# Performance work log

Measured on AMD Instinct MI355X. Metric: run time of the kernel, lower is better.

The kernel has to match this reference:

```python
import jax, jax.numpy as jnp
import numpy as np

NA, NPA, NT = 4096, 8192, 4096  # authors, papers, terms
HEADS = 8

def _ln(x, g, b):
    m = jnp.mean(x, -1, keepdims=True)
    v = jnp.var(x, -1, keepdims=True)
    return (x - m) * jax.lax.rsqrt(v + 1e-5) * g + b

def _gat(x_src, x_dst, src, dst, W, a_s, a_d, b, n_dst):
    # PyG-style GATConv (shared lin for src/dst, no self loops), per edge type.
    heads, outc = a_s.shape
    h_s = (x_src @ W).reshape(-1, heads, outc)
    h_d = (x_dst @ W).reshape(-1, heads, outc)
    e = jax.nn.leaky_relu(jnp.sum(h_s * a_s, -1)[src] + jnp.sum(h_d * a_d, -1)[dst], 0.2)  # [E,H]
    m = jax.ops.segment_max(e, dst, num_segments=n_dst)
    m = jnp.where(jnp.isfinite(m), m, 0.0)
    w = jnp.exp(e - m[dst])
    den = jax.ops.segment_sum(w, dst, num_segments=n_dst)
    alpha = w / (den[dst] + 1e-16)
    out = jax.ops.segment_sum(h_s[src] * alpha[..., None], dst, num_segments=n_dst)
    return out.reshape(n_dst, heads * outc) + b

def _gtl(x, peQ, peK, db, Wq, bq, Wk, bk, Wv, bv, Wo, bo, g1, be1, Wf1, bf1, Wf2, bf2, g2, be2):
    # PE-modulated dense multi-head attention + FFN, pre/post LN residual blocks.
    N, D = x.shape
    dh = D // HEADS
    Q = (x @ Wq + bq + peQ).reshape(N, HEADS, dh)
    K = (x @ Wk + bk + peK).reshape(N, HEADS, dh)
    V = (x @ Wv + bv).reshape(N, HEADS, dh)
    s = jnp.einsum('nhd,mhd->hnm', Q, K) / jnp.sqrt(jnp.float32(dh)) + db[None, None, :]
    o = jnp.einsum('hnm,mhd->nhd', jax.nn.softmax(s, -1), V).reshape(N, D) @ Wo + bo
    x = _ln(x + o, g1, be1)
    f = jax.nn.relu(x @ Wf1 + bf1) @ Wf2 + bf2
    return _ln(x + f, g2, be2)

def _forward(F, I):
    (x_author, x_paper, x_term, original_A, t1_W, t1_b, t2_W, t2_b, t3_W, t3_b,
     gat1_W, gat1_as, gat1_ad, gat1_b, gat2_W, gat2_as, gat2_ad, gat2_b,
     pe_embed, peWQ, peWK,
     gt_Wq, gt_bq, gt_Wk, gt_bk, gt_Wv, gt_bv, gt_Wo, gt_bo,
     gt_g1, gt_be1, gt_Wf1, gt_bf1, gt_Wf2, gt_bf2, gt_g2, gt_be2,
     cat_W, cat_b, mlp_W1, mlp_b1, mlp_W2, mlp_b2) = F
    (ap_src, ap_dst, pa_src, pa_dst, pt_src, pt_dst, tp_src, tp_dst, deg) = I
    xa = jax.nn.relu(x_author @ t1_W + t1_b)
    xp = jax.nn.relu(x_paper @ t2_W + t2_b)
    xt = jax.nn.relu(x_term @ t3_W + t3_b)
    # to_hetero GAT layer 1 (heads=8, out=128): sum over incoming edge types, relu
    h_p1 = jax.nn.relu(_gat(xa, xp, ap_src, ap_dst, gat1_W[0], gat1_as[0], gat1_ad[0], gat1_b[0], NPA)
                       + _gat(xt, xp, tp_src, tp_dst, gat1_W[3], gat1_as[3], gat1_ad[3], gat1_b[3], NPA))
    h_a1 = jax.nn.relu(_gat(xp, xa, pa_src, pa_dst, gat1_W[1], gat1_as[1], gat1_ad[1], gat1_b[1], NA))
    # layer 2 (heads=1); only author output feeds the graph transformer
    h_a2 = _gat(h_p1, h_a1, pa_src, pa_dst, gat2_W[1], gat2_as[1], gat2_ad[1], gat2_b[1], NA)
    # learned positional encodings + adjacency reconstruction loss
    peQ = pe_embed @ peWQ
    peK = pe_embed @ peWK
    S = jax.nn.sigmoid(peQ @ peK.T)  # [NA, NA]
    loss_pe = jnp.mean((S[None] - original_A) ** 2)
    db = jnp.log(jnp.maximum(deg.astype(jnp.float32), 1.0))  # degree key bias
    x = h_a2
    outs = [x]
    for i in range(gt_Wq.shape[0]):
        x = _gtl(x, peQ, peK, db, gt_Wq[i], gt_bq[i], gt_Wk[i], gt_bk[i], gt_Wv[i], gt_bv[i],
                 gt_Wo[i], gt_bo[i], gt_g1[i], gt_be1[i], gt_Wf1[i], gt_bf1[i], gt_Wf2[i], gt_bf2[i],
                 gt_g2[i], gt_be2[i])
        outs.append(x)
    x_gt = jax.nn.relu(jnp.concatenate(outs, -1) @ cat_W + cat_b)
    logits = jax.nn.relu(x_gt @ mlp_W1 + mlp_b1) @ mlp_W2 + mlp_b2
    return loss_pe, jax.nn.softmax(logits, -1), x_gt

def setup_inputs() -> dict:
    key = jax.random.key(0)
    ks = iter(jax.random.split(key, 100))
    def rn(sh, s=1.0):
        return jax.random.normal(next(ks), sh, jnp.float32) * s
    def ri(sh, hi, lo=0):
        return jax.random.randint(next(ks), sh, lo, hi)
    d = {}
    d['x_author'] = rn((NA, 334)); d['x_paper'] = rn((NPA, 512)); d['x_term'] = rn((NT, 128))
    d['ap_src'] = ri((80000,), NA); d['ap_dst'] = ri((80000,), NPA)
    d['pa_src'] = ri((80000,), NPA); d['pa_dst'] = ri((80000,), NA)
    d['pt_src'] = ri((160000,), NPA); d['pt_dst'] = ri((160000,), NT)
    d['tp_src'] = ri((160000,), NT); d['tp_dst'] = ri((160000,), NPA)
    d['original_A'] = (jax.random.uniform(next(ks), (4, NA, NA)) < 0.005).astype(jnp.float32)
    d['deg'] = ri((NA,), 64, 1)
    p = 0.05
    d['t1_W'] = rn((334, 128), p); d['t1_b'] = jnp.zeros((128,))
    d['t2_W'] = rn((512, 128), p); d['t2_b'] = jnp.zeros((128,))
    d['t3_W'] = rn((128, 128), p); d['t3_b'] = jnp.zeros((128,))
    d['gat1_W'] = rn((4, 128, 1024), p); d['gat1_as'] = rn((4, 8, 128), p)
    d['gat1_ad'] = rn((4, 8, 128), p); d['gat1_b'] = jnp.zeros((4, 1024))
    d['gat2_W'] = rn((4, 1024, 128), p); d['gat2_as'] = rn((4, 1, 128), p)
    d['gat2_ad'] = rn((4, 1, 128), p); d['gat2_b'] = jnp.zeros((4, 128))
    d['pe_embed'] = rn((NA, 128), p); d['peWQ'] = rn((128, 128), p); d['peWK'] = rn((128, 128), p)
    d['gt_Wq'] = rn((2, 128, 128), p); d['gt_bq'] = jnp.zeros((2, 128))
    d['gt_Wk'] = rn((2, 128, 128), p); d['gt_bk'] = jnp.zeros((2, 128))
    d['gt_Wv'] = rn((2, 128, 128), p); d['gt_bv'] = jnp.zeros((2, 128))
    d['gt_Wo'] = rn((2, 128, 128), p); d['gt_bo'] = jnp.zeros((2, 128))
    d['gt_g1'] = jnp.ones((2, 128)); d['gt_be1'] = jnp.zeros((2, 128))
    d['gt_Wf1'] = rn((2, 128, 256), p); d['gt_bf1'] = jnp.zeros((2, 256))
    d['gt_Wf2'] = rn((2, 256, 128), p); d['gt_bf2'] = jnp.zeros((2, 128))
    d['gt_g2'] = jnp.ones((2, 128)); d['gt_be2'] = jnp.zeros((2, 128))
    d['cat_W'] = rn((384, 128), p); d['cat_b'] = jnp.zeros((128,))
    d['mlp_W1'] = rn((128, 256), p); d['mlp_b1'] = jnp.zeros((256,))
    d['mlp_W2'] = rn((256, 4), p); d['mlp_b2'] = jnp.zeros((4,))
    return d

def reference(x_author, x_paper, x_term, ap_src, ap_dst, pa_src, pa_dst, pt_src, pt_dst, tp_src, tp_dst, original_A, deg, t1_W, t1_b, t2_W, t2_b, t3_W, t3_b, gat1_W, gat1_as, gat1_ad, gat1_b, gat2_W, gat2_as, gat2_ad, gat2_b, pe_embed, peWQ, peWK, gt_Wq, gt_bq, gt_Wk, gt_bk, gt_Wv, gt_bv, gt_Wo, gt_bo, gt_g1, gt_be1, gt_Wf1, gt_bf1, gt_Wf2, gt_bf2, gt_g2, gt_be2, cat_W, cat_b, mlp_W1, mlp_b1, mlp_W2, mlp_b2):
    F = (x_author, x_paper, x_term, original_A, t1_W, t1_b, t2_W, t2_b, t3_W, t3_b,
         gat1_W, gat1_as, gat1_ad, gat1_b, gat2_W, gat2_as, gat2_ad, gat2_b,
         pe_embed, peWQ, peWK,
         gt_Wq, gt_bq, gt_Wk, gt_bk, gt_Wv, gt_bv, gt_Wo, gt_bo,
         gt_g1, gt_be1, gt_Wf1, gt_bf1, gt_Wf2, gt_bf2, gt_g2, gt_be2,
         cat_W, cat_b, mlp_W1, mlp_b1, mlp_W2, mlp_b2)
    I = (ap_src, ap_dst, pa_src, pa_dst, pt_src, pt_dst, tp_src, tp_dst, deg)
    return _forward(F, I)
```

## Files before the change

kernel.cpp:

```cpp
#include <hip/hip_runtime.h>
#include <math.h>

#define NA   4096
#define NPA  8192
#define NT   4096
#define E_AP 80000
#define E_PA 80000
#define E_TP 160000
#define E_TOT (E_AP + E_TP + E_PA)
#define NSLOT (NPA + NPA + NA)
#define ASPLIT 4

typedef __attribute__((ext_vector_type(4))) float f32x4;
typedef __attribute__((ext_vector_type(8))) short s16x8;
typedef __attribute__((ext_vector_type(8))) unsigned short u16x8;
typedef unsigned short ushort_t;

__device__ __forceinline__ ushort_t f2bf(float f){
  unsigned u = __float_as_uint(f);
  unsigned r = u + 0x7fffu + ((u >> 16) & 1u);
  return (ushort_t)(r >> 16);
}
__device__ __forceinline__ float bf2f(ushort_t u){
  return __uint_as_float(((unsigned)u) << 16);
}

__global__ __launch_bounds__(256) void gemm_sm4_k(
    const float* __restrict__ A, const float* __restrict__ B, float* __restrict__ C,
    const float* __restrict__ bias, const float* __restrict__ lossAcc, float* __restrict__ lossOut,
    int M, int N, int K, int lda, int ldb, int ldc)
{
  if (blockIdx.x == 0 && threadIdx.x == 0)
    lossOut[0] = lossAcc[0] * (1.0f / 67108864.0f);
  __shared__ float As[16][68];
  __shared__ float Bs[16][68];
  int bm = blockIdx.x * 64, bn = 0;
  int tid = threadIdx.x;
  int tr = tid >> 4, tc = tid & 15;
  float acc[4][4] = {{0.f}};
  for (int k0 = 0; k0 < K; k0 += 16) {
#pragma unroll
    for (int i = 0; i < 4; ++i) {
      int idx = tid + i * 256;
      int r  = idx >> 4, kk = idx & 15;
      int gr = bm + r, gk = k0 + kk;
      As[kk][r] = (gr < M && gk < K) ? A[(size_t)gr * lda + gk] : 0.f;
      int c  = idx & 63, k2 = idx >> 6;
      int gc = bn + c, gk2 = k0 + k2;
      Bs[k2][c] = (gk2 < K && gc < N) ? B[(size_t)gk2 * ldb + gc] : 0.f;
    }
    __syncthreads();
#pragma unroll
    for (int kk = 0; kk < 16; ++kk) {
      float a0[4], b0[4];
#pragma unroll
      for (int i = 0; i < 4; ++i) a0[i] = As[kk][tr * 4 + i];
#pragma unroll
      for (int j = 0; j < 4; ++j) b0[j] = Bs[kk][tc * 4 + j];
#pragma unroll
      for (int i = 0; i < 4; ++i)
#pragma unroll
        for (int j = 0; j < 4; ++j) acc[i][j] = fmaf(a0[i], b0[j], acc[i][j]);
    }
    __syncthreads();
  }
  if (tc != 0) return;
#pragma unroll
  for (int i = 0; i < 4; ++i) {
    int r = bm + tr * 4 + i;
    if (r >= M) continue;
    float l0 = acc[i][0] + bias[0], l1 = acc[i][1] + bias[1];
    float l2 = acc[i][2] + bias[2], l3 = acc[i][3] + bias[3];
    float mx = fmaxf(fmaxf(l0, l1), fmaxf(l2, l3));
    float e0 = __expf(l0 - mx), e1 = __expf(l1 - mx), e2 = __expf(l2 - mx), e3 = __expf(l3 - mx);
    float inv = 1.f / (e0 + e1 + e2 + e3);
    C[(size_t)r * ldc + 0] = e0 * inv;
    C[(size_t)r * ldc + 1] = e1 * inv;
    C[(size_t)r * ldc + 2] = e2 * inv;
    C[(size_t)r * ldc + 3] = e3 * inv;
  }
}

template<int ACT, int TN>
__global__ __launch_bounds__(256) void gemm_mfma_k(
    const void* __restrict__ Ain, const void* __restrict__ A2in, const void* __restrict__ A3in,
    int aBf16,
    const float* __restrict__ B, void* __restrict__ Cout, int cBf16,
    const float* __restrict__ bias,
    const float* __restrict__ addmat, int addCols, int addLd,
    const float* __restrict__ lng, const float* __restrict__ lnb,
    const float* __restrict__ partIn,
    int M, int N, int K, int lda, int ldb, int ldc)
{
  const char* A  = (const char*)Ain;
  const char* A2 = (const char*)A2in;
  const char* A3 = (const char*)A3in;
  char* C = (char*)Cout;

  __shared__ __align__(16) ushort_t As[64][40];
  __shared__ __align__(16) ushort_t Bs[TN][40];
  constexpr int NJ = TN / 32;
  int bm = blockIdx.x * 64, bn = blockIdx.y * TN;
  int tid = threadIdx.x;
  int w = tid >> 6, lane = tid & 63, lg = lane >> 4, lid = lane & 15;
  int wm = (w & 1) * 32, wn = (w >> 1) * (TN / 2);
  f32x4 acc[2][NJ];
#pragma unroll
  for (int i = 0; i < 2; ++i)
#pragma unroll
    for (int j = 0; j < NJ; ++j) acc[i][j] = (f32x4){0.f, 0.f, 0.f, 0.f};

  for (int k0 = 0; k0 < K; k0 += 32) {
    {
      int r = tid >> 2, ks = (tid & 3) * 8;
      u16x8 v;
      if (partIn) {
        int row = bm + r;
        int kcol = k0 + ks;
        int h = kcol >> 4, d0 = kcol & 15;
        float mm = -1e30f;
#pragma unroll
        for (int sp = 0; sp < ASPLIT; ++sp)
          mm = fmaxf(mm, partIn[((size_t)(sp * 8 + h) * NA + row) * 18 + 16]);
        float ll = 0.f;
        float a[8];
#pragma unroll
        for (int j = 0; j < 8; ++j) a[j] = 0.f;
#pragma unroll
        for (int sp = 0; sp < ASPLIT; ++sp) {
          const float* pp = partIn + ((size_t)(sp * 8 + h) * NA + row) * 18;
          float wq = __expf(pp[16] - mm);
          ll += pp[17] * wq;
#pragma unroll
          for (int j = 0; j < 8; ++j) a[j] = fmaf(pp[d0 + j], wq, a[j]);
        }
        float inv = 1.f / ll;
#pragma unroll
        for (int j = 0; j < 8; ++j) v[j] = f2bf(a[j] * inv);
      } else {
        int kcol = k0 + ks;
        const char* Ab = A;
        if (A2) { int seg = kcol >> 7; Ab = (seg == 0) ? A : ((seg == 1) ? A2 : A3); kcol &= 127; }
        if (aBf16) {
          v = *(const u16x8*)((const ushort_t*)Ab + (size_t)(bm + (tid >> 2)) * lda + kcol);
        } else {
          const float* ap = (const float*)Ab + (size_t)(bm + (tid >> 2)) * lda + kcol;
#pragma unroll
          for (int j = 0; j < 8; ++j) {
            int gk = k0 + ks + j;
            float fv = (gk < K) ? ap[j] : 0.f;
            v[j] = f2bf(fv);
          }
        }
      }
      *(u16x8*)&As[tid >> 2][ks] = v;
    }
    if (TN == 128) {
      int n = tid >> 1, ks = (tid & 1) * 16;
      ushort_t tmp[16];
#pragma unroll
      for (int j = 0; j < 16; ++j) {
        int gk = k0 + ks + j;
        float fv = (gk < K) ? B[(size_t)gk * ldb + bn + n] : 0.f;
        tmp[j] = f2bf(fv);
      }
      u16x8 v0, v1;
#pragma unroll
      for (int j = 0; j < 8; ++j) { v0[j] = tmp[j]; v1[j] = tmp[8 + j]; }
      *(u16x8*)&Bs[n][ks] = v0;
      *(u16x8*)&Bs[n][ks + 8] = v1;
// ... 9 lines not shown
      *(u16x8*)&Bs[n][ks] = v;
    }
    __syncthreads();
    s16x8 a_frag[2], b_frag[NJ];
#pragma unroll
    for (int i = 0; i < 2; ++i) a_frag[i] = *(s16x8*)&As[wm + i * 16 + lid][lg * 8];
#pragma unroll
    for (int j = 0; j < NJ; ++j) b_frag[j] = *(s16x8*)&Bs[wn + j * 16 + lid][lg * 8];
#pragma unroll
    for (int i = 0; i < 2; ++i)
#pragma unroll
      for (int j = 0; j < NJ; ++j)
        acc[i][j] = __builtin_amdgcn_mfma_f32_16x16x32_bf16(a_frag[i], b_frag[j], acc[i][j], 0, 0, 0);
    __syncthreads();
  }
  if (ACT == 2) {
    __shared__ float Ct[64][132];
#pragma unroll
    for (int i = 0; i < 2; ++i) {
#pragma unroll
      for (int j = 0; j < NJ; ++j) {
        int coll = wn + j * 16 + lid;
#pragma unroll
        for (int rr = 0; rr < 4; ++rr) {
          int rowl = wm + i * 16 + lg * 4 + rr;
          float v = acc[i][j][rr];
          if (bias) v += bias[coll];
          if (addmat && coll < addCols) v += addmat[(size_t)(bm + rowl) * addLd + coll];
          Ct[rowl][coll] = v;
        }
      }
// ... 6 lines not shown
      float v = Ct[row][part * 32 + c2];
      s += v; q += v * v;
    }
    s += __shfl_xor(s, 1); q += __shfl_xor(q, 1);
    s += __shfl_xor(s, 2); q += __shfl_xor(q, 2);
    float mean = s * (1.f / 128.f);
    float var = q * (1.f / 128.f) - mean * mean;
    float inv = rsqrtf(var + 1e-5f);
    int r = bm + row;
    float* Cf = (float*)C;
#pragma unroll
    for (int c2 = 0; c2 < 32; ++c2) {
      int c = part * 32 + c2;
      Cf[(size_t)r * ldc + c] = (Ct[row][c] - mean) * inv * lng[c] + lnb[c];
    }
  } else {
#pragma unroll
    for (int i = 0; i < 2; ++i) {
#pragma unroll
      for (int j = 0; j < NJ; ++j) {
        int c = bn + wn + j * 16 + lid;
#pragma unroll
        for (int rr = 0; rr < 4; ++rr) {
          int r = bm + wm + i * 16 + lg * 4 + rr;
          float v = acc[i][j][rr];
          if (bias)   v += bias[c];
          if (addmat && c < addCols) v += addmat[(size_t)r * addLd + c];
          if (ACT == 1) v = fmaxf(v, 0.f);
          if (cBf16) ((ushort_t*)C)[(size_t)r * ldc + c] = f2bf(v);
          else       ((float*)C)[(size_t)r * ldc + c] = v;
// ... 104 lines not shown
        else       ((float*)C)[(size_t)r * ldc + c] = v;
      }
    }
  }
}

__global__ void prep_k(const float* __restrict__ gat1_b, const float* __restrict__ gat1_W,
                       const float* __restrict__ Wq, const float* __restrict__ bq,
                       const float* __restrict__ Wk, const float* __restrict__ bk,
                       const float* __restrict__ Wv, const float* __restrict__ bv,
                       const float* __restrict__ peWQ, const float* __restrict__ peWK,
                       const int* __restrict__ deg,
                       const float* __restrict__ gat1_as, const float* __restrict__ gat1_ad,
                       const int* __restrict__ ap_dst, const int* __restrict__ tp_dst,
                       const int* __restrict__ pa_dst,
                       float* __restrict__ bsum, float* __restrict__ Wqkv,
                       float* __restrict__ bqkv, float* __restrict__ peW,
                       float* __restrict__ Bstack, float* __restrict__ dbv,
                       float* __restrict__ Ps, float* __restrict__ Pd,
                       int* __restrict__ cnt)
{
  int idx = blockIdx.x * blockDim.x + threadIdx.x;
  if (idx < 1024) { bsum[idx] = gat1_b[idx] + gat1_b[3 * 1024 + idx]; return; }
  idx -= 1024;
  if (idx < 2 * 128 * 384) {
    int l = idx / 49152, rem = idx % 49152;
    int k = rem / 384, c = rem % 384;
    float v;
    if (c < 128)      v = Wq[(size_t)l * 16384 + k * 128 + c];
    else if (c < 256) v = Wk[(size_t)l * 16384 + k * 128 + c - 128];
    else              v = Wv[(size_t)l * 16384 + k * 128 + c - 256];
    Wqkv[(size_t)l * 49152 + k * 384 + c] = v;
    return;
  }
  idx -= 2 * 128 * 384;
// ... 30 lines not shown
    const float* a1 = gat1_as + wsel[type] * 1024 + h * 128;
    const float* a2 = gat1_ad + wsel[type] * 1024 + h * 128;
    float s1 = 0.f, s2 = 0.f;
    for (int c = 0; c < 128; ++c){ float wv = wr[c]; s1 = fmaf(wv, a1[c], s1); s2 = fmaf(wv, a2[c], s2); }
    Ps[(size_t)type * 1024 + k * 8 + h] = s1;
    Pd[(size_t)type * 1024 + k * 8 + h] = s2;
    return;
  }
  idx -= 3 * 1024;
  if (idx < E_TOT) {
    int slot;
    if (idx < E_AP)             slot = ap_dst[idx];
    else if (idx < E_AP + E_TP) slot = NPA + tp_dst[idx - E_AP];
    else                        slot = 2 * NPA + pa_dst[idx - E_AP - E_TP];
    atomicAdd(&cnt[slot], 1);
  }
}

__global__ void scatterf_k(const int* __restrict__ ap_dst, const int* __restrict__ tp_dst,
                           const int* __restrict__ pa_dst, const int* __restrict__ off,
                           int* __restrict__ cur, int* __restrict__ eidx){
  int i = blockIdx.x * blockDim.x + threadIdx.x;
  if (i >= E_TOT) return;
  int slot, local;
  if (i < E_AP)             { local = i;                 slot = ap_dst[local]; }
  else if (i < E_AP + E_TP) { local = i - E_AP;          slot = NPA + tp_dst[local]; }
  else                      { local = i - E_AP - E_TP;   slot = 2 * NPA + pa_dst[local]; }
  int p = atomicAdd(&cur[slot], 1);
  eidx[off[slot] + p] = local;
}
// ... 129 lines not shown
    float mn = fmaxf(mh, v);
    float sc = __expf(mh - mn);
    float w_ = __expf(v - mn);
    den = den * sc + w_;
    mh = mn;
    unsigned u = *(const unsigned*)(hs + (size_t)s * 128 + 2 * lane);
    a0 = fmaf(w_, bf2f((ushort_t)(u & 0xffff)), a0 * sc);
    a1 = fmaf(w_, bf2f((ushort_t)(u >> 16)), a1 * sc);
    e = en; s = sn;
  }
  float inv = 1.f / (den + 1e-16f);
  outp[(size_t)d * 128 + 2 * lane]     = a0 * inv + bias[2 * lane];
  outp[(size_t)d * 128 + 2 * lane + 1] = a1 * inv + bias[2 * lane + 1];
}

__global__ __launch_bounds__(256) void rowdot2_k(const ushort_t* __restrict__ X,
    const float* __restrict__ va, const float* __restrict__ vb, float* __restrict__ out){
  int r = blockIdx.x * 4 + (threadIdx.x >> 6);
  int lane = threadIdx.x & 63;
  const float* v = (r < 8192) ? va : vb;
  unsigned u = *(const unsigned*)(X + (size_t)r * 128 + 2 * lane);
  float s = bf2f((ushort_t)(u & 0xffff)) * v[2 * lane]
          + bf2f((ushort_t)(u >> 16)) * v[2 * lane + 1];
#pragma unroll
  for (int o = 32; o; o >>= 1) s += __shfl_down(s, o);
  if (lane == 0) out[r] = s;
}

__global__ __launch_bounds__(256) void loss_mfma_k(const float* __restrict__ peQ,
    const float* __restrict__ peK, const float* __restrict__ A4, float* __restrict__ lossAcc)
{
  __shared__ __align__(16) ushort_t As[64][40];
  __shared__ __align__(16) ushort_t Bs[128][40];
  __shared__ float sig[64][128];
  __shared__ float red[256];
  int br = blockIdx.x * 64, bc = blockIdx.y * 128;
  int tid = threadIdx.x;
  int w = tid >> 6, lane = tid & 63, lg = lane >> 4, lid = lane & 15;
  int wm = (w & 1) * 32, wn = (w >> 1) * 64;
  f32x4 acc[2][4];
#pragma unroll
  for (int i = 0; i < 2; ++i)
#pragma unroll
// ... 154 lines not shown
      s16x8 pa = *(s16x8*)&Pl[w][lid][32 * kc + 8 * lg];
      s16x8 vb = *(s16x8*)&Vt[lid][32 * kc + 8 * lg];
      o = __builtin_amdgcn_mfma_f32_16x16x32_bf16(pa, vb, o, 0, 0, 0);
    }
  }
  float* pb = part + ((size_t)(sp * 8 + h) * NA) * 18;
#pragma unroll
  for (int r = 0; r < 4; ++r) {
    int qq = qbase + 16 * w + 4 * lg + r;
    pb[(size_t)qq * 18 + lid] = o[r];
  }
  if (lg == 0) {
    int qq = qbase + 16 * w + lid;
    pb[(size_t)qq * 18 + 16] = m;
    pb[(size_t)qq * 18 + 17] = l;
  }
}

__global__ void setval_k(float* p, float v){ p[0] = v; }

extern "C" void kernel_launch(void* const* d_in, const int* in_sizes, int n_in,
                              void* d_out, int out_size, void* d_ws, size_t ws_size,
                              hipStream_t stream)
{
  (void)in_sizes; (void)n_in; (void)out_size;
  const float* x_author = (const float*)d_in[0];
  const float* x_paper  = (const float*)d_in[1];
  const float* x_term   = (const float*)d_in[2];
  const int* ap_src = (const int*)d_in[3];
  const int* ap_dst = (const int*)d_in[4];
// ... 45 lines not shown
  ushort_t* agg  = (ushort_t*)alloc((size_t)NSLOT * 1024 * 2);
  float* scores = (float*)alloc((size_t)36864 * 8 * 4);
  float* Ps   = (float*)alloc(3 * 1024 * 4);
  float* Pd   = (float*)alloc(3 * 1024 * 4);
  ushort_t* hs2 = (ushort_t*)alloc((size_t)NPA * 128 * 2);
  ushort_t* hd2 = (ushort_t*)alloc((size_t)NA * 128 * 2);
  float* s2sd = (float*)alloc((size_t)(NPA + NA) * 4);
  float* hA2  = (float*)alloc((size_t)NA * 128 * 4);
  float* peQK = (float*)alloc((size_t)NA * 256 * 4);
  float* dbv  = (float*)alloc((size_t)NA * 4);
  float* bsum = (float*)alloc(1024 * 4);
  float* Wqkv = (float*)alloc((size_t)2 * 128 * 384 * 4);
  float* bqkv = (float*)alloc((size_t)2 * 384 * 4);
  float* peW  = (float*)alloc((size_t)128 * 256 * 4);
  float* Bstack = (float*)alloc((size_t)256 * 1024 * 4);
  ushort_t* QKVb = (ushort_t*)alloc((size_t)NA * 384 * 2);
  float* x1b  = (float*)alloc((size_t)NA * 128 * 4);
  ushort_t* f1 = (ushort_t*)alloc((size_t)NA * 256 * 2);
  float* outs1= (float*)alloc((size_t)NA * 128 * 4);
  float* outs2= (float*)alloc((size_t)NA * 128 * 4);
  float* l1   = (float*)alloc((size_t)NA * 256 * 4);
  int*   offb = (int*)alloc((size_t)NSLOT * 4);
  int*   eidx = (int*)alloc((size_t)E_TOT * 4);
  size_t zstart = off;
  int*      cnt   = (int*)alloc((size_t)NSLOT * 4);
  int*      cur   = (int*)alloc((size_t)NSLOT * 4);
  float*    lossAcc = (float*)alloc(256);
  size_t zlen = off - zstart;

  float* part = (float*)accP;

  if (off > ws_size){
    setval_k<<<1, 1, 0, stream>>>(out, -12345.0f);
    return;
  }

  auto gemmx = [&](int act, int tn, const void* A, const void* A2, const void* A3, int aBf16,
                   const float* B, void* C, int cBf16, const float* bias,
                   const float* addmat, int addCols, int addLd,
                   const float* lng, const float* lnb, const float* partIn,
                   int M, int N, int K, int lda, int ldb, int ldc){
    dim3 g(M / 64, N / tn, 1);
    if (tn == 128) {
      if (act == 0)      gemm_mfma_k<0,128><<<g, 256, 0, stream>>>(A, A2, A3, aBf16, B, C, cBf16, bias, addmat, addCols, addLd, lng, lnb, partIn, M, N, K, lda, ldb, ldc);
      else if (act == 1) gemm_mfma_k<1,128><<<g, 256, 0, stream>>>(A, A2, A3, aBf16, B, C, cBf16, bias, addmat, addCols, addLd, lng, lnb, partIn, M, N, K, lda, ldb, ldc);
      else               gemm_mfma_k<2,128><<<g, 256, 0, stream>>>(A, A2, A3, aBf16, B, C, cBf16, bias, addmat, addCols, addLd, lng, lnb, partIn, M, N, K, lda, ldb, ldc);
    } else {
      if (act == 0)      gemm_mfma_k<0,64><<<g, 256, 0, stream>>>(A, A2, A3, aBf16, B, C, cBf16, bias, addmat, addCols, addLd, lng, lnb, partIn, M, N, K, lda, ldb, ldc);
      else               gemm_mfma_k<1,64><<<g, 256, 0, stream>>>(A, A2, A3, aBf16, B, C, cBf16, bias, addmat, addCols, addLd, lng, lnb, partIn, M, N, K, lda, ldb, ldc);
    }
  };

  hipMemsetAsync(base + zstart, 0, zlen, stream);
  prep_k<<<2822, 256, 0, stream>>>(gat1_b, gat1_W, gt_Wq, gt_bq, gt_Wk, gt_bk, gt_Wv, gt_bv,
                                   peWQ, peWK, deg, gat1_as, gat1_ad, ap_dst, tp_dst, pa_dst,
                                   bsum, Wqkv, bqkv, peW, Bstack, dbv, Ps, Pd, cnt);
  {
    GDescArr da; da.nd = 4;
    da.d[0] = { x_author, nullptr, t1_W, xa, t1_b, 0, 1, 1, NA, 128, 334, 334, 128, 128, 1, 0, 0, 0, 0 };
    da.d[1] = { x_paper,  nullptr, t2_W, xp, t2_b, 0, 1, 1, NPA, 128, 512, 512, 128, 128, 1, 0, 0, 0, 128 };
    da.d[2] = { x_term,   nullptr, t3_W, xt, t3_b, 0, 1, 1, NT, 128, 128, 128, 128, 128, 1, 0, 0, 0, 384 };
    da.d[3] = { pe_embed, nullptr, peW, peQK, nullptr, 0, 0, 0, NA, 256, 128, 128, 256, 256, 1, 0, 0, 0, 512 };
    gemm_multi_k<<<768, 256, 0, stream>>>(da);
  }
  exscan_k<<<1, 1024, 0, stream>>>(cnt, offb, NSLOT);
  scatterf_k<<<(E_TOT + 255) / 256, 256, 0, stream>>>(ap_dst, tp_dst, pa_dst, offb, cur, eidx);
  scorev_k<<<9216, 256, 0, stream>>>(xa, xp, xt, Ps, Pd, scores);
  agg8ff_k<<<NSLOT / 4, 256, 0, stream>>>(eidx, offb, cnt, ap_src, tp_src, pa_src,
                                          xa, xt, xp, scores, agg);
  {
    GDescArr da; da.nd = 2;
    da.d[0] = { agg, agg + (size_t)NPA * 1024, Bstack, accP, bsum, 1, 1, 1,
                NPA, 128, 256, 1024, 1024, 1024, 8, 128, 128, 128, 0 };
    da.d[1] = { agg + (size_t)2 * NPA * 1024, nullptr, gat1_W + 131072, accA, gat1_b + 1024, 1, 1, 1,
                NA, 128, 128, 1024, 1024, 1024, 8, 128, 128, 128, 2048 };
    gemm_multi_k<<<3072, 256, 0, stream>>>(da);
  }
  gemmx(0, 64, accP, 0, 0, 1, gat2_W + 131072, hs2, 1, 0, 0, 0, 0, 0, 0, 0,
        NPA + NA, 128, 1024, 1024, 128, 128);
  rowdot2_k<<<(NPA + NA) / 4, 256, 0, stream>>>(hs2, gat2_as + 128, gat2_ad + 128, s2sd);
  gat_agg1f_k<<<NA / 4, 256, 0, stream>>>(eidx, offb + 2 * NPA, cnt + 2 * NPA, pa_src, hs2, s2sd,
                                          gat2_b + 128, hA2, NA);
  loss_mfma_k<<<dim3(64, 32), 256, 0, stream>>>(peQK, peQK + 128, original_A, lossAcc);
  const float* x = hA2;
  float* louts[2] = { outs1, outs2 };
  for (int i = 0; i < 2; ++i){
    const float* Wo = gt_Wo + i * 16384; const float* bo = gt_bo + i * 128;
    const float* Wf1 = gt_Wf1 + i * 32768; const float* bf1 = gt_bf1 + i * 256;
    const float* Wf2 = gt_Wf2 + i * 32768; const float* bf2 = gt_bf2 + i * 128;
    gemmx(0, 64, x, 0, 0, 0, Wqkv + (size_t)i * 49152, QKVb, 1, bqkv + i * 384, peQK, 256, 256,
          0, 0, 0, NA, 384, 128, 128, 384, 384);
    attn_mfma_k<<<dim3(NA / 64, 8, ASPLIT), 256, 0, stream>>>(QKVb, QKVb + 128, QKVb + 256, dbv, part);
    gemmx(2, 128, nullptr, 0, 0, 0, Wo, x1b, 0, bo, x, 128, 128, gt_g1 + i * 128, gt_be1 + i * 128,
          part, NA, 128, 128, 128, 128, 128);
    gemmx(1, 64, x1b, 0, 0, 0, Wf1, f1, 1, bf1, 0, 0, 0, 0, 0, 0, NA, 256, 128, 128, 256, 256);
    gemmx(2, 128, f1, 0, 0, 1, Wf2, louts[i], 0, bf2, x1b, 128, 128, gt_g2 + i * 128, gt_be2 + i * 128,
          0, NA, 128, 256, 256, 128, 128);
    x = louts[i];
  }
  float* xgt = out + 1 + NA * 4;
  gemmx(1, 64, hA2, outs1, outs2, 0, cat_W, xgt, 0, cat_b, 0, 0, 0, 0, 0, 0,
        NA, 128, 384, 128, 128, 128);
  gemmx(1, 64, xgt, 0, 0, 0, mlp_W1, l1, 0, mlp_b1, 0, 0, 0, 0, 0, 0, NA, 256, 128, 128, 256, 256);
  gemm_sm4_k<<<64, 256, 0, stream>>>(l1, mlp_W2, out + 1, mlp_b2, lossAcc, out, NA, 4, 256, 256, 4, 4);
}
```

Measured before the change: 777.4 us.

## Fuse transformer tail and MLP head into single kernels with pre-transposed bf16 weights

Each transformer layer's output projection, first LayerNorm, FFN and second LayerNorm now run in one kernel over 16-row tiles, keeping intermediates in shared memory. The concat/MLP head is fused the same way, including the final softmax. The GAT2 row-dot is folded into the GEMM epilogue, and weights are pre-transposed to bf16 in the prep kernel. This removes several launches and global round trips, at the cost of 16-row tiles that reuse weights less and launch only 256 blocks per kernel.

```diff
diff --git a/kernel.cpp b/kernel.cpp
--- a/kernel.cpp
+++ b/kernel.cpp
@@ -25,62 +25,6 @@
   return __uint_as_float(((unsigned)u) << 16);
 }
 
-__global__ __launch_bounds__(256) void gemm_sm4_k(
-    const float* __restrict__ A, const float* __restrict__ B, float* __restrict__ C,
-    const float* __restrict__ bias, const float* __restrict__ lossAcc, float* __restrict__ lossOut,
-    int M, int N, int K, int lda, int ldb, int ldc)
-{
-  if (blockIdx.x == 0 && threadIdx.x == 0)
-    lossOut[0] = lossAcc[0] * (1.0f / 67108864.0f);
-  __shared__ float As[16][68];
-  __shared__ float Bs[16][68];
-  int bm = blockIdx.x * 64, bn = 0;
-  int tid = threadIdx.x;
-  int tr = tid >> 4, tc = tid & 15;
-  float acc[4][4] = {{0.f}};
-  for (int k0 = 0; k0 < K; k0 += 16) {
-#pragma unroll
-    for (int i = 0; i < 4; ++i) {
-      int idx = tid + i * 256;
-      int r  = idx >> 4, kk = idx & 15;
-      int gr = bm + r, gk = k0 + kk;
-      As[kk][r] = (gr < M && gk < K) ? A[(size_t)gr * lda + gk] : 0.f;
-      int c  = idx & 63, k2 = idx >> 6;
-      int gc = bn + c, gk2 = k0 + k2;
-      Bs[k2][c] = (gk2 < K && gc < N) ? B[(size_t)gk2 * ldb + gc] : 0.f;
-    }
-    __syncthreads();
-#pragma unroll
-    for (int kk = 0; kk < 16; ++kk) {
-      float a0[4], b0[4];
-#pragma unroll
-      for (int i = 0; i < 4; ++i) a0[i] = As[kk][tr * 4 + i];
-#pragma unroll
-      for (int j = 0; j < 4; ++j) b0[j] = Bs[kk][tc * 4 + j];
-#pragma unroll
-      for (int i = 0; i < 4; ++i)
-#pragma unroll
-        for (int j = 0; j < 4; ++j) acc[i][j] = fmaf(a0[i], b0[j], acc[i][j]);
-    }
-    __syncthreads();
-  }
-  if (tc != 0) return;
-#pragma unroll
-  for (int i = 0; i < 4; ++i) {
-    int r = bm + tr * 4 + i;
-    if (r >= M) continue;
-    float l0 = acc[i][0] + bias[0], l1 = acc[i][1] + bias[1];
-    float l2 = acc[i][2] + bias[2], l3 = acc[i][3] + bias[3];
-    float mx = fmaxf(fmaxf(l0, l1), fmaxf(l2, l3));
-    float e0 = __expf(l0 - mx), e1 = __expf(l1 - mx), e2 = __expf(l2 - mx), e3 = __expf(l3 - mx);
-    float inv = 1.f / (e0 + e1 + e2 + e3);
-    C[(size_t)r * ldc + 0] = e0 * inv;
-    C[(size_t)r * ldc + 1] = e1 * inv;
-    C[(size_t)r * ldc + 2] = e2 * inv;
-    C[(size_t)r * ldc + 3] = e3 * inv;
-  }
-}
-
 template<int ACT, int TN>
 __global__ __launch_bounds__(256) void gemm_mfma_k(
     const void* __restrict__ Ain, const void* __restrict__ A2in, const void* __restrict__ A3in,
@@ -89,7 +33,7 @@
     const float* __restrict__ bias,
     const float* __restrict__ addmat, int addCols, int addLd,
     const float* __restrict__ lng, const float* __restrict__ lnb,
-    const float* __restrict__ partIn,
+    float* __restrict__ rdOut,
     int M, int N, int K, int lda, int ldb, int ldc)
 {
   const char* A  = (const char*)Ain;
@@ -113,47 +57,22 @@
   for (int k0 = 0; k0 < K; k0 += 32) {
     {
       int r = tid >> 2, ks = (tid & 3) * 8;
+      int kcol = k0 + ks;
+      const char* Ab = A;
+      if (A2) { int seg = kcol >> 7; Ab = (seg == 0) ? A : ((seg == 1) ? A2 : A3); kcol &= 127; }
       u16x8 v;
-      if (partIn) {
-        int row = bm + r;
-        int kcol = k0 + ks;
-        int h = kcol >> 4, d0 = kcol & 15;
-        float mm = -1e30f;
-#pragma unroll
-        for (int sp = 0; sp < ASPLIT; ++sp)
-          mm = fmaxf(mm, partIn[((size_t)(sp * 8 + h) * NA + row) * 18 + 16]);
-        float ll = 0.f;
-        float a[8];
-#pragma unroll
-        for (int j = 0; j < 8; ++j) a[j] = 0.f;
-#pragma unroll
-        for (int sp = 0; sp < ASPLIT; ++sp) {
-          const float* pp = partIn + ((size_t)(sp * 8 + h) * NA + row) * 18;
-          float wq = __expf(pp[16] - mm);
-          ll += pp[17] * wq;
-#pragma unroll
-          for (int j = 0; j < 8; ++j) a[j] = fmaf(pp[d0 + j], wq, a[j]);
-        }
-        float inv = 1.f / ll;
-#pragma unroll
-        for (int j = 0; j < 8; ++j) v[j] = f2bf(a[j] * inv);
+      if (aBf16) {
+        v = *(const u16x8*)((const ushort_t*)Ab + (size_t)(bm + r) * lda + kcol);
       } else {
-        int kcol = k0 + ks;
-        const char* Ab = A;
-        if (A2) { int seg = kcol >> 7; Ab = (seg == 0) ? A : ((seg == 1) ? A2 : A3); kcol &= 127; }
-        if (aBf16) {
-          v = *(const u16x8*)((const ushort_t*)Ab + (size_t)(bm + (tid >> 2)) * lda + kcol);
-        } else {
-          const float* ap = (const float*)Ab + (size_t)(bm + (tid >> 2)) * lda + kcol;
-#pragma unroll
-          for (int j = 0; j < 8; ++j) {
-            int gk = k0 + ks + j;
-            float fv = (gk < K) ? ap[j] : 0.f;
-            v[j] = f2bf(fv);
-          }
+        const float* ap = (const float*)Ab + (size_t)(bm + r) * lda + kcol;
+#pragma unroll
+        for (int j = 0; j < 8; ++j) {
+          int gk = k0 + ks + j;
+          float fv = (gk < K) ? ap[j] : 0.f;
+          v[j] = f2bf(fv);
         }
       }
-      *(u16x8*)&As[tid >> 2][ks] = v;
+      *(u16x8*)&As[r][ks] = v;
     }
     if (TN == 128) {
       int n = tid >> 1, ks = (tid & 1) * 16;
@@ -193,7 +112,7 @@
         acc[i][j] = __builtin_amdgcn_mfma_f32_16x16x32_bf16(a_frag[i], b_frag[j], acc[i][j], 0, 0, 0);
     __syncthreads();
   }
-  if (ACT == 2) {
+  if constexpr (ACT == 2) {
     __shared__ float Ct[64][132];
 #pragma unroll
     for (int i = 0; i < 2; ++i) {
@@ -230,6 +149,35 @@
       int c = part * 32 + c2;
       Cf[(size_t)r * ldc + c] = (Ct[row][c] - mean) * inv * lng[c] + lnb[c];
     }
+  } else if constexpr (ACT == 3) {
+    __shared__ float Ct[64][132];
+#pragma unroll
+    for (int i = 0; i < 2; ++i) {
+#pragma unroll
+      for (int j = 0; j < NJ; ++j) {
+        int coll = wn + j * 16 + lid;
+#pragma unroll
+        for (int rr = 0; rr < 4; ++rr) {
+          int rowl = wm + i * 16 + lg * 4 + rr;
+          Ct[rowl][coll] = acc[i][j][rr];
+        }
+      }
+    }
+    __syncthreads();
+    int row = tid >> 2, part = tid & 3;
+    const float* vsel = (bm + row < 8192) ? lng : lnb;
+    float rd = 0.f;
+    ushort_t* Cu = (ushort_t*)C;
+#pragma unroll
+    for (int c2 = 0; c2 < 32; ++c2) {
+      int c = part * 32 + c2;
+      float f = Ct[row][c];
+      rd = fmaf(f, vsel[c], rd);
+      Cu[(size_t)(bm + row) * ldc + c] = f2bf(f);
+    }
+    rd += __shfl_xor(rd, 1);
+    rd += __shfl_xor(rd, 2);
+    if (part == 0) rdOut[bm + row] = rd;
   } else {
 #pragma unroll
     for (int i = 0; i < 2; ++i) {
@@ -364,11 +312,17 @@
                        const float* __restrict__ gat1_as, const float* __restrict__ gat1_ad,
                        const int* __restrict__ ap_dst, const int* __restrict__ tp_dst,
                        const int* __restrict__ pa_dst,
+                       const float* __restrict__ gt_Wo, const float* __restrict__ gt_Wf1,
+                       const float* __restrict__ gt_Wf2, const float* __restrict__ cat_W,
+                       const float* __restrict__ mlp_W1,
                        float* __restrict__ bsum, float* __restrict__ Wqkv,
                        float* __restrict__ bqkv, float* __restrict__ peW,
                        float* __restrict__ Bstack, float* __restrict__ dbv,
                        float* __restrict__ Ps, float* __restrict__ Pd,
-                       int* __restrict__ cnt)
+                       int* __restrict__ cnt,
+                       ushort_t* __restrict__ Wot, ushort_t* __restrict__ Wf1t,
+                       ushort_t* __restrict__ Wf2t, ushort_t* __restrict__ catt,
+                       ushort_t* __restrict__ mlp1t)
 {
   int idx = blockIdx.x * blockDim.x + threadIdx.x;
   if (idx < 1024) { bsum[idx] = gat1_b[idx] + gat1_b[3 * 1024 + idx]; return; }
@@ -429,6 +383,39 @@
     else if (idx < E_AP + E_TP) slot = NPA + tp_dst[idx - E_AP];
     else                        slot = 2 * NPA + pa_dst[idx - E_AP - E_TP];
     atomicAdd(&cnt[slot], 1);
+    return;
+  }
+  idx -= E_TOT;
+  if (idx < 2 * 128 * 128) {
+    int l = idx / 16384, rem = idx % 16384;
+    int n = rem / 128, k = rem % 128;
+    Wot[idx] = f2bf(gt_Wo[(size_t)l * 16384 + k * 128 + n]);
+    return;
+  }
+  idx -= 2 * 128 * 128;
+  if (idx < 2 * 256 * 128) {
+    int l = idx / 32768, rem = idx % 32768;
+    int n = rem / 128, k = rem % 128;
+    Wf1t[idx] = f2bf(gt_Wf1[(size_t)l * 32768 + k * 256 + n]);
+    return;
+  }
+  idx -= 2 * 256 * 128;
+  if (idx < 2 * 128 * 256) {
+    int l = idx / 32768, rem = idx % 32768;
+    int n = rem / 256, k = rem % 256;
+    Wf2t[idx] = f2bf(gt_Wf2[(size_t)l * 32768 + k * 128 + n]);
+    return;
+  }
+  idx -= 2 * 128 * 256;
+  if (idx < 128 * 384) {
+    int n = idx / 384, k = idx % 384;
+    catt[idx] = f2bf(cat_W[(size_t)k * 128 + n]);
+    return;
+  }
+  idx -= 128 * 384;
+  if (idx < 256 * 128) {
+    int n = idx / 128, k = idx % 128;
+    mlp1t[idx] = f2bf(mlp_W1[(size_t)k * 256 + n]);
   }
 }
 
@@ -588,19 +575,6 @@
   outp[(size_t)d * 128 + 2 * lane + 1] = a1 * inv + bias[2 * lane + 1];
 }
 
-__global__ __launch_bounds__(256) void rowdot2_k(const ushort_t* __restrict__ X,
-    const float* __restrict__ va, const float* __restrict__ vb, float* __restrict__ out){
-  int r = blockIdx.x * 4 + (threadIdx.x >> 6);
-  int lane = threadIdx.x & 63;
-  const float* v = (r < 8192) ? va : vb;
-  unsigned u = *(const unsigned*)(X + (size_t)r * 128 + 2 * lane);
-  float s = bf2f((ushort_t)(u & 0xffff)) * v[2 * lane]
-          + bf2f((ushort_t)(u >> 16)) * v[2 * lane + 1];
-#pragma unroll
-  for (int o = 32; o; o >>= 1) s += __shfl_down(s, o);
-  if (lane == 0) out[r] = s;
-}
-
 __global__ __launch_bounds__(256) void loss_mfma_k(const float* __restrict__ peQ,
     const float* __restrict__ peK, const float* __restrict__ A4, float* __restrict__ lossAcc)
 {
@@ -785,6 +759,270 @@
     int qq = qbase + 16 * w + lid;
     pb[(size_t)qq * 18 + 16] = m;
     pb[(size_t)qq * 18 + 17] = l;
+  }
+}
+
+__global__ __launch_bounds__(256) void gt_tail_k(
+    const float* __restrict__ part,
+    const ushort_t* __restrict__ Wot, const float* __restrict__ bo,
+    const float* __restrict__ xin,
+    const float* __restrict__ g1, const float* __restrict__ be1,
+    const ushort_t* __restrict__ Wf1t, const float* __restrict__ bf1,
+    const ushort_t* __restrict__ Wf2t, const float* __restrict__ bf2,
+    const float* __restrict__ g2, const float* __restrict__ be2,
+    float* __restrict__ outX)
+{
+  __shared__ __align__(16) ushort_t Aly[16][136];
+  __shared__ __align__(16) ushort_t Bs[256][40];
+  __shared__ __align__(16) ushort_t F1b[16][264];
+  __shared__ float X1[16][132];
+  int bm = blockIdx.x * 16;
+  int tid = threadIdx.x;
+  int w = tid >> 6, lane = tid & 63, lg = lane >> 4, lid = lane & 15;
+
+  {
+    int row = bm + (tid >> 4);
+    int seg = tid & 15;
+    int kcol = seg * 8;
+    int h = kcol >> 4, d0 = kcol & 15;
+    float mm = -1e30f;
+#pragma unroll
+    for (int sp = 0; sp < ASPLIT; ++sp)
+      mm = fmaxf(mm, part[((size_t)(sp * 8 + h) * NA + row) * 18 + 16]);
+    float ll = 0.f, a[8];
+#pragma unroll
+    for (int j = 0; j < 8; ++j) a[j] = 0.f;
+#pragma unroll
+    for (int sp = 0; sp < ASPLIT; ++sp){
+      const float* pp = part + ((size_t)(sp * 8 + h) * NA + row) * 18;
+      float wq = __expf(pp[16] - mm);
+      ll += pp[17] * wq;
+#pragma unroll
+      for (int j = 0; j < 8; ++j) a[j] = fmaf(pp[d0 + j], wq, a[j]);
+    }
+    float inv = 1.f / ll;
+    u16x8 v;
+#pragma unroll
+    for (int j = 0; j < 8; ++j) v[j] = f2bf(a[j] * inv);
+    *(u16x8*)&Aly[tid >> 4][kcol] = v;
+  }
+  __syncthreads();
+
+  f32x4 acc1[2];
+  acc1[0] = (f32x4){0.f,0.f,0.f,0.f};
+  acc1[1] = (f32x4){0.f,0.f,0.f,0.f};
+  for (int k0 = 0; k0 < 128; k0 += 32){
+    int n = tid >> 1, ks = (tid & 1) * 16;
+    *(u16x8*)&Bs[n][ks]     = *(const u16x8*)(Wot + (size_t)n * 128 + k0 + ks);
+    *(u16x8*)&Bs[n][ks + 8] = *(const u16x8*)(Wot + (size_t)n * 128 + k0 + ks + 8);
+    __syncthreads();
+    s16x8 af = *(s16x8*)&Aly[lid][k0 + lg * 8];
+#pragma unroll
+    for (int j = 0; j < 2; ++j){
+      s16x8 bf = *(s16x8*)&Bs[w * 32 + j * 16 + lid][lg * 8];
+      acc1[j] = __builtin_amdgcn_mfma_f32_16x16x32_bf16(af, bf, acc1[j], 0, 0, 0);
+    }
+    __syncthreads();
+  }
+#pragma unroll
+  for (int j = 0; j < 2; ++j)
+#pragma unroll
+    for (int rr = 0; rr < 4; ++rr){
+      int r = lg * 4 + rr, c = w * 32 + j * 16 + lid;
+      X1[r][c] = acc1[j][rr] + bo[c] + xin[(size_t)(bm + r) * 128 + c];
+    }
+  __syncthreads();
+  {
+    int r = tid >> 4, p = tid & 15;
+    float s = 0.f, q = 0.f;
+#pragma unroll
+    for (int j = 0; j < 8; ++j){ float v = X1[r][p * 8 + j]; s += v; q += v * v; }
+#pragma unroll
+    for (int mk = 1; mk < 16; mk <<= 1){ s += __shfl_xor(s, mk); q += __shfl_xor(q, mk); }
+    float mean = s * (1.f / 128.f), var = q * (1.f / 128.f) - mean * mean;
+    float inv = rsqrtf(var + 1e-5f);
+    u16x8 v;
+#pragma unroll
+    for (int j = 0; j < 8; ++j){
+      int c = p * 8 + j;
+      float f = (X1[r][c] - mean) * inv * g1[c] + be1[c];
+      X1[r][c] = f;
+      v[j] = f2bf(f);
+    }
+    *(u16x8*)&Aly[r][p * 8] = v;
+  }
+  __syncthreads();
+
+  f32x4 acc2[4];
+#pragma unroll
+  for (int j = 0; j < 4; ++j) acc2[j] = (f32x4){0.f,0.f,0.f,0.f};
+  for (int k0 = 0; k0 < 128; k0 += 32){
+#pragma unroll
+    for (int q4 = 0; q4 < 4; ++q4)
+      *(u16x8*)&Bs[tid][q4 * 8] = *(const u16x8*)(Wf1t + (size_t)tid * 128 + k0 + q4 * 8);
+    __syncthreads();
+    s16x8 af = *(s16x8*)&Aly[lid][k0 + lg * 8];
+#pragma unroll
+    for (int j = 0; j < 4; ++j){
+      s16x8 bf = *(s16x8*)&Bs[w * 64 + j * 16 + lid][lg * 8];
+      acc2[j] = __builtin_amdgcn_mfma_f32_16x16x32_bf16(af, bf, acc2[j], 0, 0, 0);
+    }
+    __syncthreads();
+  }
+#pragma unroll
+  for (int j = 0; j < 4; ++j)
+#pragma unroll
+    for (int rr = 0; rr < 4; ++rr){
+      int r = lg * 4 + rr, c = w * 64 + j * 16 + lid;
+      F1b[r][c] = f2bf(fmaxf(acc2[j][rr] + bf1[c], 0.f));
+    }
+  __syncthreads();
+
+  f32x4 acc3[2];
+  acc3[0] = (f32x4){0.f,0.f,0.f,0.f};
+  acc3[1] = (f32x4){0.f,0.f,0.f,0.f};
+  for (int k0 = 0; k0 < 256; k0 += 32){
+    int n = tid >> 1, ks = (tid & 1) * 16;
+    *(u16x8*)&Bs[n][ks]     = *(const u16x8*)(Wf2t + (size_t)n * 256 + k0 + ks);
+    *(u16x8*)&Bs[n][ks + 8] = *(const u16x8*)(Wf2t + (size_t)n * 256 + k0 + ks + 8);
+    __syncthreads();
+    s16x8 af = *(s16x8*)&F1b[lid][k0 + lg * 8];
+#pragma unroll
+    for (int j = 0; j < 2; ++j){
+      s16x8 bf = *(s16x8*)&Bs[w * 32 + j * 16 + lid][lg * 8];
+      acc3[j] = __builtin_amdgcn_mfma_f32_16x16x32_bf16(af, bf, acc3[j], 0, 0, 0);
+    }
+    __syncthreads();
+  }
+#pragma unroll
+  for (int j = 0; j < 2; ++j)
+#pragma unroll
+    for (int rr = 0; rr < 4; ++rr){
+      int r = lg * 4 + rr, c = w * 32 + j * 16 + lid;
+      X1[r][c] = acc3[j][rr] + bf2[c] + X1[r][c];
+    }
+  __syncthreads();
+  {
+    int r = tid >> 4, p = tid & 15;
+    float s = 0.f, q = 0.f;
+#pragma unroll
+    for (int j = 0; j < 8; ++j){ float v = X1[r][p * 8 + j]; s += v; q += v * v; }
+#pragma unroll
+    for (int mk = 1; mk < 16; mk <<= 1){ s += __shfl_xor(s, mk); q += __shfl_xor(q, mk); }
+    float mean = s * (1.f / 128.f), var = q * (1.f / 128.f) - mean * mean;
+    float inv = rsqrtf(var + 1e-5f);
+#pragma unroll
+    for (int j = 0; j < 8; ++j){
+      int c = p * 8 + j;
+      outX[(size_t)(bm + r) * 128 + c] = (X1[r][c] - mean) * inv * g2[c] + be2[c];
+    }
+  }
+}
+
+__global__ __launch_bounds__(256) void head_k(
+    const float* __restrict__ hA2, const float* __restrict__ o1, const float* __restrict__ o2,
+    const ushort_t* __restrict__ catt, const float* __restrict__ cat_b,
+    const ushort_t* __restrict__ mlp1t, const float* __restrict__ mlp_b1,
+    const float* __restrict__ mlp_W2, const float* __restrict__ mlp_b2,
+    const float* __restrict__ lossAcc, float* __restrict__ out)
+{
+  __shared__ __align__(16) ushort_t Aly[16][392];
+  __shared__ __align__(16) ushort_t Bs[256][40];
+  __shared__ __align__(16) ushort_t L1b[16][264];
+  __shared__ float LG[16][4];
+  int bm = blockIdx.x * 16;
+  int tid = threadIdx.x;
+  int w = tid >> 6, lane = tid & 63, lg = lane >> 4, lid = lane & 15;
+  if (blockIdx.x == 0 && tid == 0) out[0] = lossAcc[0] * (1.0f / 67108864.0f);
+
+  {
+    int r = bm + (tid >> 4), seg = tid & 15;
+#pragma unroll
+    for (int ch = 0; ch < 3; ++ch){
+      int c0 = seg * 24 + ch * 8;
+      const float* src; int cc;
+      if (c0 < 128)      { src = hA2; cc = c0; }
+      else if (c0 < 256) { src = o1;  cc = c0 - 128; }
+      else               { src = o2;  cc = c0 - 256; }
+      u16x8 v;
+#pragma unroll
+      for (int j = 0; j < 8; ++j) v[j] = f2bf(src[(size_t)r * 128 + cc + j]);
+      *(u16x8*)&Aly[tid >> 4][c0] = v;
+    }
+  }
+  __syncthreads();
+
+  float* xgt = out + 1 + NA * 4;
+  f32x4 acc1[2];
+  acc1[0] = (f32x4){0.f,0.f,0.f,0.f};
+  acc1[1] = (f32x4){0.f,0.f,0.f,0.f};
+  for (int k0 = 0; k0 < 384; k0 += 32){
+    int n = tid >> 1, ks = (tid & 1) * 16;
+    *(u16x8*)&Bs[n][ks]     = *(const u16x8*)(catt + (size_t)n * 384 + k0 + ks);
+    *(u16x8*)&Bs[n][ks + 8] = *(const u16x8*)(catt + (size_t)n * 384 + k0 + ks + 8);
+    __syncthreads();
+    s16x8 af = *(s16x8*)&Aly[lid][k0 + lg * 8];
+#pragma unroll
+    for (int j = 0; j < 2; ++j){
+      s16x8 bf = *(s16x8*)&Bs[w * 32 + j * 16 + lid][lg * 8];
+      acc1[j] = __builtin_amdgcn_mfma_f32_16x16x32_bf16(af, bf, acc1[j], 0, 0, 0);
+    }
+    __syncthreads();
+  }
+#pragma unroll
+  for (int j = 0; j < 2; ++j)
+#pragma unroll
+    for (int rr = 0; rr < 4; ++rr){
+      int r = lg * 4 + rr, c = w * 32 + j * 16 + lid;
+      float f = fmaxf(acc1[j][rr] + cat_b[c], 0.f);
+      xgt[(size_t)(bm + r) * 128 + c] = f;
+      Aly[r][c] = f2bf(f);
+    }
+  __syncthreads();
+
+  f32x4 acc2[4];
+#pragma unroll
+  for (int j = 0; j < 4; ++j) acc2[j] = (f32x4){0.f,0.f,0.f,0.f};
+  for (int k0 = 0; k0 < 128; k0 += 32){
+#pragma unroll
+    for (int q4 = 0; q4 < 4; ++q4)
+      *(u16x8*)&Bs[tid][q4 * 8] = *(const u16x8*)(mlp1t + (size_t)tid * 128 + k0 + q4 * 8);
+    __syncthreads();
+    s16x8 af = *(s16x8*)&Aly[lid][k0 + lg * 8];
+#pragma unroll
+    for (int j = 0; j < 4; ++j){
+      s16x8 bf = *(s16x8*)&Bs[w * 64 + j * 16 + lid][lg * 8];
+      acc2[j] = __builtin_amdgcn_mfma_f32_16x16x32_bf16(af, bf, acc2[j], 0, 0, 0);
+    }
+    __syncthreads();
+  }
+#pragma unroll
+  for (int j = 0; j < 4; ++j)
+#pragma unroll
+    for (int rr = 0; rr < 4; ++rr){
+      int r = lg * 4 + rr, c = w * 64 + j * 16 + lid;
+      L1b[r][c] = f2bf(fmaxf(acc2[j][rr] + mlp_b1[c], 0.f));
+    }
+  __syncthreads();
+
+  {
+    int r = tid >> 4, rem = tid & 15, c = rem >> 2, p = rem & 3;
+    float s = 0.f;
+    for (int k = p * 64; k < p * 64 + 64; ++k)
+      s = fmaf(bf2f(L1b[r][k]), mlp_W2[(size_t)k * 4 + c], s);
+    s += __shfl_xor(s, 1);
+    s += __shfl_xor(s, 2);
+    if (p == 0) LG[r][c] = s + mlp_b2[c];
+  }
+  __syncthreads();
+  if (tid < 16){
+    int r = tid;
+    float l0 = LG[r][0], l1 = LG[r][1], l2 = LG[r][2], l3 = LG[r][3];
+    float mx = fmaxf(fmaxf(l0, l1), fmaxf(l2, l3));
+    float e0 = __expf(l0 - mx), e1 = __expf(l1 - mx), e2 = __expf(l2 - mx), e3 = __expf(l3 - mx);
+    float inv = 1.f / (e0 + e1 + e2 + e3);
+    float* o = out + 1 + (size_t)(bm + r) * 4;
+    o[0] = e0 * inv; o[1] = e1 * inv; o[2] = e2 * inv; o[3] = e3 * inv;
   }
 }
 
@@ -860,12 +1098,14 @@
   float* bqkv = (float*)alloc((size_t)2 * 384 * 4);
   float* peW  = (float*)alloc((size_t)128 * 256 * 4);
   float* Bstack = (float*)alloc((size_t)256 * 1024 * 4);
+  ushort_t* Wot   = (ushort_t*)alloc((size_t)2 * 128 * 128 * 2);
+  ushort_t* Wf1t  = (ushort_t*)alloc((size_t)2 * 256 * 128 * 2);
+  ushort_t* Wf2t  = (ushort_t*)alloc((size_t)2 * 128 * 256 * 2);
+  ushort_t* catt  = (ushort_t*)alloc((size_t)128 * 384 * 2);
+  ushort_t* mlp1t = (ushort_t*)alloc((size_t)256 * 128 * 2);
   ushort_t* QKVb = (ushort_t*)alloc((size_t)NA * 384 * 2);
-  float* x1b  = (float*)alloc((size_t)NA * 128 * 4);
-  ushort_t* f1 = (ushort_t*)alloc((size_t)NA * 256 * 2);
   float* outs1= (float*)alloc((size_t)NA * 128 * 4);
   float* outs2= (float*)alloc((size_t)NA * 128 * 4);
-  float* l1   = (float*)alloc((size_t)NA * 256 * 4);
   int*   offb = (int*)alloc((size_t)NSLOT * 4);
   int*   eidx = (int*)alloc((size_t)E_TOT * 4);
   size_t zstart = off;
@@ -884,23 +1124,26 @@
   auto gemmx = [&](int act, int tn, const void* A, const void* A2, const void* A3, int aBf16,
                    const float* B, void* C, int cBf16, const float* bias,
                    const float* addmat, int addCols, int addLd,
-                   const float* lng, const float* lnb, const float* partIn,
+                   const float* lng, const float* lnb, float* rdOut,
                    int M, int N, int K, int lda, int ldb, int ldc){
     dim3 g(M / 64, N / tn, 1);
     if (tn == 128) {
-      if (act == 0)      gemm_mfma_k<0,128><<<g, 256, 0, stream>>>(A, A2, A3, aBf16, B, C, cBf16, bias, addmat, addCols, addLd, lng, lnb, partIn, M, N, K, lda, ldb, ldc);
-      else if (act == 1) gemm_mfma_k<1,128><<<g, 256, 0, stream>>>(A, A2, A3, aBf16, B, C, cBf16, bias, addmat, addCols, addLd, lng, lnb, partIn, M, N, K, lda, ldb, ldc);
-      else               gemm_mfma_k<2,128><<<g, 256, 0, stream>>>(A, A2, A3, aBf16, B, C, cBf16, bias, addmat, addCols, addLd, lng, lnb, partIn, M, N, K, lda, ldb, ldc);
+      if (act == 0)      gemm_mfma_k<0,128><<<g, 256, 0, stream>>>(A, A2, A3, aBf16, B, C, cBf16, bias, addmat, addCols, addLd, lng, lnb, rdOut, M, N, K, lda, ldb, ldc);
+      else if (act == 1) gemm_mfma_k<1,128><<<g, 256, 0, stream>>>(A, A2, A3, aBf16, B, C, cBf16, bias, addmat, addCols, addLd, lng, lnb, rdOut, M, N, K, lda, ldb, ldc);
+      else if (act == 2) gemm_mfma_k<2,128><<<g, 256, 0, stream>>>(A, A2, A3, aBf16, B, C, cBf16, bias, addmat, addCols, addLd, lng, lnb, rdOut, M, N, K, lda, ldb, ldc);
+      else               gemm_mfma_k<3,128><<<g, 256, 0, stream>>>(A, A2, A3, aBf16, B, C, cBf16, bias, addmat, addCols, addLd, lng, lnb, rdOut, M, N, K, lda, ldb, ldc);
     } else {
-      if (act == 0)      gemm_mfma_k<0,64><<<g, 256, 0, stream>>>(A, A2, A3, aBf16, B, C, cBf16, bias, addmat, addCols, addLd, lng, lnb, partIn, M, N, K, lda, ldb, ldc);
-      else               gemm_mfma_k<1,64><<<g, 256, 0, stream>>>(A, A2, A3, aBf16, B, C, cBf16, bias, addmat, addCols, addLd, lng, lnb, partIn, M, N, K, lda, ldb, ldc);
+      if (act == 0)      gemm_mfma_k<0,64><<<g, 256, 0, stream>>>(A, A2, A3, aBf16, B, C, cBf16, bias, addmat, addCols, addLd, lng, lnb, rdOut, M, N, K, lda, ldb, ldc);
+      else               gemm_mfma_k<1,64><<<g, 256, 0, stream>>>(A, A2, A3, aBf16, B, C, cBf16, bias, addmat, addCols, addLd, lng, lnb, rdOut, M, N, K, lda, ldb, ldc);
     }
   };
 
   hipMemsetAsync(base + zstart, 0, zlen, stream);
-  prep_k<<<2822, 256, 0, stream>>>(gat1_b, gat1_W, gt_Wq, gt_bq, gt_Wk, gt_bk, gt_Wv, gt_bv,
+  prep_k<<<3781, 256, 0, stream>>>(gat1_b, gat1_W, gt_Wq, gt_bq, gt_Wk, gt_bk, gt_Wv, gt_bv,
                                    peWQ, peWK, deg, gat1_as, gat1_ad, ap_dst, tp_dst, pa_dst,
-                                   bsum, Wqkv, bqkv, peW, Bstack, dbv, Ps, Pd, cnt);
+                                   gt_Wo, gt_Wf1, gt_Wf2, cat_W, mlp_W1,
+                                   bsum, Wqkv, bqkv, peW, Bstack, dbv, Ps, Pd, cnt,
+                                   Wot, Wf1t, Wf2t, catt, mlp1t);
   {
     GDescArr da; da.nd = 4;
     da.d[0] = { x_author, nullptr, t1_W, xa, t1_b, 0, 1, 1, NA, 128, 334, 334, 128, 128, 1, 0, 0, 0, 0 };
@@ -922,31 +1165,24 @@
                 NA, 128, 128, 1024, 1024, 1024, 8, 128, 128, 128, 2048 };
     gemm_multi_k<<<3072, 256, 0, stream>>>(da);
   }
-  gemmx(0, 64, accP, 0, 0, 1, gat2_W + 131072, hs2, 1, 0, 0, 0, 0, 0, 0, 0,
-        NPA + NA, 128, 1024, 1024, 128, 128);
-  rowdot2_k<<<(NPA + NA) / 4, 256, 0, stream>>>(hs2, gat2_as + 128, gat2_ad + 128, s2sd);
+  gemmx(3, 128, accP, 0, 0, 1, gat2_W + 131072, hs2, 1, 0, 0, 0, 0,
+        gat2_as + 128, gat2_ad + 128, s2sd, NPA + NA, 128, 1024, 1024, 128, 128);
   gat_agg1f_k<<<NA / 4, 256, 0, stream>>>(eidx, offb + 2 * NPA, cnt + 2 * NPA, pa_src, hs2, s2sd,
                                           gat2_b + 128, hA2, NA);
   loss_mfma_k<<<dim3(64, 32), 256, 0, stream>>>(peQK, peQK + 128, original_A, lossAcc);
   const float* x = hA2;
   float* louts[2] = { outs1, outs2 };
   for (int i = 0; i < 2; ++i){
-    const float* Wo = gt_Wo + i * 16384; const float* bo = gt_bo + i * 128;
-    const float* Wf1 = gt_Wf1 + i * 32768; const float* bf1 = gt_bf1 + i * 256;
-    const float* Wf2 = gt_Wf2 + i * 32768; const float* bf2 = gt_bf2 + i * 128;
     gemmx(0, 64, x, 0, 0, 0, Wqkv + (size_t)i * 49152, QKVb, 1, bqkv + i * 384, peQK, 256, 256,
           0, 0, 0, NA, 384, 128, 128, 384, 384);
     attn_mfma_k<<<dim3(NA / 64, 8, ASPLIT), 256, 0, stream>>>(QKVb, QKVb + 128, QKVb + 256, dbv, part);
-    gemmx(2, 128, nullptr, 0, 0, 0, Wo, x1b, 0, bo, x, 128, 128, gt_g1 + i * 128, gt_be1 + i * 128,
-          part, NA, 128, 128, 128, 128, 128);
-    gemmx(1, 64, x1b, 0, 0, 0, Wf1, f1, 1, bf1, 0, 0, 0, 0, 0, 0, NA, 256, 128, 128, 256, 256);
-    gemmx(2, 128, f1, 0, 0, 1, Wf2, louts[i], 0, bf2, x1b, 128, 128, gt_g2 + i * 128, gt_be2 + i * 128,
-          0, NA, 128, 256, 256, 128, 128);
+    gt_tail_k<<<NA / 16, 256, 0, stream>>>(part, Wot + (size_t)i * 16384, gt_bo + i * 128, x,
+                                           gt_g1 + i * 128, gt_be1 + i * 128,
+                                           Wf1t + (size_t)i * 32768, gt_bf1 + i * 256,
+                                           Wf2t + (size_t)i * 32768, gt_bf2 + i * 128,
+                                           gt_g2 + i * 128, gt_be2 + i * 128, louts[i]);
     x = louts[i];
   }
-  float* xgt = out + 1 + NA * 4;
-  gemmx(1, 64, hA2, outs1, outs2, 0, cat_W, xgt, 0, cat_b, 0, 0, 0, 0, 0, 0,
-        NA, 128, 384, 128, 128, 128);
-  gemmx(1, 64, xgt, 0, 0, 0, mlp_W1, l1, 0, mlp_b1, 0, 0, 0, 0, 0, 0, NA, 256, 128, 128, 256, 256);
-  gemm_sm4_k<<<64, 256, 0, stream>>>(l1, mlp_W2, out + 1, mlp_b2, lossAcc, out, NA, 4, 256, 256, 4, 4);
-}
+  head_k<<<NA / 16, 256, 0, stream>>>(hA2, outs1, outs2, catt, cat_b, mlp1t, mlp_b1,
+                                      mlp_W2, mlp_b2, lossAcc, out);
+}
```

Result: faster. 646.2 us (-16.9%).
